# Kernel tuning notes

Measured on AMD Instinct MI355X. Metric: run time of the kernel, lower is better.

The kernel has to match this reference:

```python
import jax, jax.numpy as jnp
import numpy as np

NM = 16  # n_modes


def setup_inputs() -> dict:
    key = jax.random.key(0)
    k1, k2, k3, k4 = jax.random.split(key, 4)
    B, M, N, I, O = 8, 256, 256, 64, 64
    std = 1.0 / (I * O)
    x = jax.random.normal(k1, (B, M, N, I), dtype=jnp.float32)
    w1 = jax.random.normal(k2, (I, O, NM, NM, 2), dtype=jnp.float32) * std
    w2 = jax.random.normal(k3, (I, O, NM, NM, 2), dtype=jnp.float32) * std
    lin_w = jax.random.normal(k4, (O, O), dtype=jnp.float32) * (1.0 / np.sqrt(O))
    lin_b = jnp.zeros((O,), dtype=jnp.float32)
    return {"x": x, "w1": w1, "w2": w2, "lin_w": lin_w, "lin_b": lin_b}


def _to_complex(w):
    return jax.lax.complex(w[..., 0], w[..., 1])


def reference(x, w1, w2, lin_w, lin_b):
    B, M, N, I = x.shape
    O = w1.shape[1]
    # [B, I, M, N]
    xt = jnp.transpose(x, (0, 3, 1, 2))
    # rfft over last two dims -> [B, I, M, N//2 + 1] complex
    x_ft = jnp.fft.rfft2(xt, s=(M, N), axes=(-2, -1))
    w1c = _to_complex(w1)  # [I, O, NM, NM]
    w2c = _to_complex(w2)
    # truncated complex matmuls over low modes (top rows) and high-negative modes (bottom rows)
    out_top = jnp.einsum('bixy,ioxy->boxy', x_ft[:, :, :NM, :NM], w1c)
    out_bot = jnp.einsum('bixy,ioxy->boxy', x_ft[:, :, -NM:, :NM], w2c)
    zeros_mid = jnp.zeros((B, O, M - 2 * NM, NM), dtype=out_top.dtype)
    rows = jnp.concatenate([out_top, zeros_mid, out_bot], axis=2)  # [B, O, M, NM]
    zeros_right = jnp.zeros((B, O, M, N // 2 + 1 - NM), dtype=out_top.dtype)
    out_ft = jnp.concatenate([rows, zeros_right], axis=3)  # [B, O, M, N//2+1]
    y = jnp.fft.irfft2(out_ft, s=(M, N), axes=(-2, -1))  # real [B, O, M, N]
    y = jnp.transpose(y, (0, 2, 3, 1))  # [B, M, N, O]
    res = y @ lin_w + lin_b
    return jax.nn.relu(y + res)
```

## Files before the change

### kernel.cpp

```cpp
#include <hip/hip_runtime.h>
#include <hip/hip_bf16.h>
#include <math.h>


#define TOFF  65536
#define XOFF  (TOFF + 4194304)
#define YOFF  (XOFF + 524288)
#define GOFF  (YOFF + 524288)

__global__ __launch_bounds__(256) void setup_tables(const float* __restrict__ lin_w,
                                                    float* __restrict__ ws) {
    int j = blockIdx.x * 256 + threadIdx.x;
    const float ANG = 0.024543692606170259f;
    if (j < 4096) {
        int n = j >> 4, ky = j & 15;
        int a = (n * ky) & 255;
        float s, c; sincosf(ANG * (float)a, &s, &c);
        float* p = ws + n * 32 + ky * 2;
        p[0] = c; p[1] = -s;
    } else if (j < 12288) {
        int e = j - 4096; int m = e >> 5, kx = e & 31;
        int kxe = kx + (kx < 16 ? 0 : 224);
        int a = (m * kxe) & 255;
        float s, c; sincosf(ANG * (float)a, &s, &c);
        int g = kx >> 2, kl = kx & 3;
        float* p = ws + 8192 + g * 2048 + m * 8 + kl * 2;
        p[0] = c; p[1] = -s;
    } else if (j < 20480) {
        int e = j - 12288; int kx = e >> 8, m = e & 255;
        int kxe = kx + (kx < 16 ? 0 : 224);
        int a = (kxe * m) & 255;
        float s, c; sincosf(ANG * (float)a, &s, &c);
        float* p = ws + 24576 + (kx * 256 + m) * 2;
        p[0] = c * (1.0f / 256.0f);
        p[1] = s * (1.0f / 256.0f);
    } else if (j < 28672) {
        int e = j - 20480; int f = e >> 8, n = e & 255;
        int ky = f >> 1, h = f & 1;
        int a = (ky * n) & 255;
        float s, c; sincosf(ANG * (float)a, &s, &c);
        float scale = (ky == 0 ? 1.0f : 2.0f) * (1.0f / 256.0f);
        ws[40960 + f * 256 + n] = h ? (-scale * s) : (scale * c);
    } else if (j < 32768) {
        int e = j - 28672;
        int op = e >> 6, o = e & 63;
        ws[49152 + e] = lin_w[e] + ((op == o) ? 1.0f : 0.0f);
    }
}

__global__ __launch_bounds__(256) void stageA(const float* __restrict__ x,
                                              const float* __restrict__ tabA,
                                              float* __restrict__ T) {
    __shared__ float red[2 * 8 * 64 * 2];
    int bid = blockIdx.x;
    int b = bid >> 8, m = bid & 255;
    int t = threadIdx.x;
    int i = t & 63, w = t >> 6;
    int kh = w & 1, h = w >> 1;
    const float* xp = x + (size_t)bid * 16384 + (size_t)h * 8192 + i;
    const float* twp = tabA + __builtin_amdgcn_readfirstlane(h * 4096 + kh * 16);
    float aR[8], aI[8];
#pragma unroll
    for (int j = 0; j < 8; ++j) { aR[j] = 0.f; aI[j] = 0.f; }
#pragma unroll 4
    for (int nn = 0; nn < 128; ++nn) {
        float xv = xp[nn * 64];
        const float* tp = twp + nn * 32;
#pragma unroll
        for (int j = 0; j < 8; ++j) {
            aR[j] = fmaf(tp[2 * j], xv, aR[j]);
            aI[j] = fmaf(tp[2 * j + 1], xv, aI[j]);
        }
    }
    float2* rp = (float2*)red + (kh * 8) * 64 + i;
    if (h == 1) {
#pragma unroll
        for (int j = 0; j < 8; ++j) rp[j * 64] = make_float2(aR[j], aI[j]);
    }
    __syncthreads();
    if (h == 0) {
        float2* Tb = (float2*)T;
#pragma unroll
        for (int j = 0; j < 8; ++j) {
            float2 p = rp[j * 64];
            int ky = kh * 8 + j;
            Tb[((size_t)(b * 16 + ky) * 256 + m) * 64 + i] =
                make_float2(aR[j] + p.x, aI[j] + p.y);
        }
    }
}

__global__ __launch_bounds__(512) void stageB(const float* __restrict__ T,
                                              const float* __restrict__ twF,
                                              float* __restrict__ X) {
    __shared__ float red[4 * 4 * 64 * 2];
    int bid = blockIdx.x;
    int b = bid >> 5;
    int ky = (bid >> 1) & 15;
    int half = bid & 1;
    int t = threadIdx.x, i = t & 63;
    int q = (t >> 6) & 3, h = t >> 8;
    int Q = half * 4 + q;
    const float2* Tp = (const float2*)T + (size_t)(b * 16 + ky) * 256 * 64 + i;
    const float* tw = twF + __builtin_amdgcn_readfirstlane(Q * 2048);
    float r0 = 0, r1 = 0, r2 = 0, r3 = 0;
    float s0 = 0, s1 = 0, s2 = 0, s3 = 0;
    int m0 = h * 128;
#pragma unroll 4
    for (int mm = 0; mm < 128; ++mm) {
        int m = m0 + mm;
        float2 tv = Tp[(size_t)m * 64];
        const float* tp = tw + m * 8;
        r0 = fmaf(tv.x, tp[0], fmaf(-tv.y, tp[1], r0));
        s0 = fmaf(tv.x, tp[1], fmaf( tv.y, tp[0], s0));
        r1 = fmaf(tv.x, tp[2], fmaf(-tv.y, tp[3], r1));
        s1 = fmaf(tv.x, tp[3], fmaf( tv.y, tp[2], s1));
        r2 = fmaf(tv.x, tp[4], fmaf(-tv.y, tp[5], r2));
        s2 = fmaf(tv.x, tp[5], fmaf( tv.y, tp[4], s2));
        r3 = fmaf(tv.x, tp[6], fmaf(-tv.y, tp[7], r3));
        s3 = fmaf(tv.x, tp[7], fmaf( tv.y, tp[6], s3));
    }
    float2* rp = (float2*)red + (q * 4) * 64 + i;
    if (h == 1) {
        rp[0 * 64] = make_float2(r0, s0);
        rp[1 * 64] = make_float2(r1, s1);
        rp[2 * 64] = make_float2(r2, s2);
        rp[3 * 64] = make_float2(r3, s3);
    }
    __syncthreads();
    if (h == 0) {
        float2 p0 = rp[0 * 64], p1 = rp[1 * 64], p2 = rp[2 * 64], p3 = rp[3 * 64];
        r0 += p0.x; s0 += p0.y; r1 += p1.x; s1 += p1.y;
        r2 += p2.x; s2 += p2.y; r3 += p3.x; s3 += p3.y;
        int kx0 = Q * 4;
        float2* Xb = (float2*)X;
        size_t base = ((size_t)(b * 16 + ky) * 32 + kx0) * 64 + i;
        Xb[base + 0 * 64] = make_float2(r0, s0);
        Xb[base + 1 * 64] = make_float2(r1, s1);
        Xb[base + 2 * 64] = make_float2(r2, s2);
        Xb[base + 3 * 64] = make_float2(r3, s3);
    }
}

__global__ __launch_bounds__(256) void stageC(const float* __restrict__ Xg,
                                              const float* __restrict__ w1,
                                              const float* __restrict__ w2,
                                              const float* __restrict__ Wf,
                                              float* __restrict__ Y2) {
    __shared__ float Ws[64 * 64 * 2];
    __shared__ float Xs[8 * 64 * 2];
    __shared__ float Ys[8 * 64 * 2];
    __shared__ float Wfs[64 * 64];
    int bid = blockIdx.x;
    int kx = bid & 31, ky = bid >> 5;
    int t = threadIdx.x;
    const float* wsrc = (kx < 16) ? w1 : w2;
    int xx = kx & 15;
#pragma unroll
    for (int q = 0; q < 16; ++q) {
        int p = t + q * 256;
        int ii = p >> 6, oo = p & 63;
        float2 wv = *(const float2*)(wsrc + ((size_t)(ii * 64 + oo) * 256 + xx * 16 + ky) * 2);
        ((float2*)Ws)[ii * 64 + oo] = wv;
    }
#pragma unroll
    for (int q = 0; q < 2; ++q) {
        int p = t + q * 256;
        int bb = p >> 6, ii = p & 63;
        ((float2*)Xs)[bb * 64 + ii] =
            ((const float2*)Xg)[((size_t)(bb * 16 + ky) * 32 + kx) * 64 + ii];
    }
#pragma unroll
    for (int q = 0; q < 16; ++q) Wfs[t + q * 256] = Wf[t + q * 256];
    __syncthreads();
    int o = t & 63, bg = t >> 6;
    float yr0 = 0, yi0 = 0, yr1 = 0, yi1 = 0;
    for (int ii = 0; ii < 64; ++ii) {
        float2 w = ((float2*)Ws)[ii * 64 + o];
        float2 xa = ((float2*)Xs)[bg * 64 + ii];
        float2 xb = ((float2*)Xs)[(bg + 4) * 64 + ii];
        yr0 = fmaf(xa.x, w.x, fmaf(-xa.y, w.y, yr0));
        yi0 = fmaf(xa.x, w.y, fmaf( xa.y, w.x, yi0));
        yr1 = fmaf(xb.x, w.x, fmaf(-xb.y, w.y, yr1));
        yi1 = fmaf(xb.x, w.y, fmaf( xb.y, w.x, yi1));
    }
    ((float2*)Ys)[bg * 64 + o] = make_float2(yr0, yi0);
    ((float2*)Ys)[(bg + 4) * 64 + o] = make_float2(yr1, yi1);
    __syncthreads();
    float zr0 = 0, zi0 = 0, zr1 = 0, zi1 = 0;
    for (int op = 0; op < 64; ++op) {
        float wf = Wfs[op * 64 + o];
        float2 ya = ((float2*)Ys)[bg * 64 + op];
        float2 yb = ((float2*)Ys)[(bg + 4) * 64 + op];
        zr0 = fmaf(ya.x, wf, zr0); zi0 = fmaf(ya.y, wf, zi0);
        zr1 = fmaf(yb.x, wf, zr1); zi1 = fmaf(yb.y, wf, zi1);
    }
    float2* Yb = (float2*)Y2;
    Yb[((size_t)(bg * 32 + kx) * 16 + ky) * 64 + o] = make_float2(zr0, zi0);
    Yb[((size_t)((bg + 4) * 32 + kx) * 16 + ky) * 64 + o] = make_float2(zr1, zi1);
}

__global__ __launch_bounds__(512) void stageD(const float* __restrict__ Y2,
                                              const float* __restrict__ twI,
                                              float* __restrict__ G) {
    __shared__ float Ysl[16 * 64 * 2];
    int bid = blockIdx.x;
    int b = bid >> 5, mg = bid & 31;
    int t = threadIdx.x, o = t & 63, ml = t >> 6;
    int m = mg * 8 + ml;
    float gr[16], gi[16];
#pragma unroll
    for (int k = 0; k < 16; ++k) { gr[k] = 0.f; gi[k] = 0.f; }
    for (int kx = 0; kx < 32; ++kx) {
        __syncthreads();
        const float2* src = (const float2*)Y2 + (size_t)(b * 32 + kx) * 1024;
#pragma unroll
        for (int qq = 0; qq < 2; ++qq) ((float2*)Ysl)[t + qq * 512] = src[t + qq * 512];
        __syncthreads();
        int off = __builtin_amdgcn_readfirstlane((kx * 256 + m) * 2);
        float c = twI[off], d = twI[off + 1];
#pragma unroll
        for (int ky = 0; ky < 16; ++ky) {
            float2 yv = ((float2*)Ysl)[ky * 64 + o];
            gr[ky] = fmaf(yv.x, c, fmaf(-yv.y, d, gr[ky]));
            gi[ky] = fmaf(yv.x, d, fmaf( yv.y, c, gi[ky]));
        }
    }
    float2* Gb = (float2*)G;
#pragma unroll
    for (int ky = 0; ky < 16; ++ky)
        Gb[((size_t)(b * 256 + m) * 16 + ky) * 64 + o] = make_float2(gr[ky], gi[ky]);
}

__global__ __launch_bounds__(256) void stageE(const float* __restrict__ G,
                                              const float* __restrict__ tabE,
                                              const float* __restrict__ lin_b,
                                              float* __restrict__ out) {
    __shared__ float Bs[32 * 256];
    __shared__ float Hs[32 * 64];
    int bid = blockIdx.x;
    int t = threadIdx.x;
    const float4* tE4 = (const float4*)tabE;
#pragma unroll
    for (int q = 0; q < 8; ++q) ((float4*)Bs)[t + q * 256] = tE4[t + q * 256];
    const float2* Gp = (const float2*)G + (size_t)bid * 1024;
#pragma unroll
    for (int q = 0; q < 4; ++q) {
        int p = t + q * 256;
        int ky = p >> 6, o = p & 63;
        float2 g = Gp[p];
        Hs[(2 * ky) * 64 + o] = g.x;
        Hs[(2 * ky + 1) * 64 + o] = g.y;
    }
    __syncthreads();
    int o4 = (t & 15) * 4, n0 = (t >> 4) * 16;
    float acc[16][4];
#pragma unroll
    for (int j = 0; j < 16; ++j) { acc[j][0] = acc[j][1] = acc[j][2] = acc[j][3] = 0.f; }
    for (int f = 0; f < 32; ++f) {
        float4 h = *(const float4*)(Hs + f * 64 + o4);
        const float* bp = Bs + f * 256 + n0;
        float4 a0 = *(const float4*)(bp);
        float4 a1 = *(const float4*)(bp + 4);
        float4 a2 = *(const float4*)(bp + 8);
        float4 a3 = *(const float4*)(bp + 12);
        float av[16] = {a0.x, a0.y, a0.z, a0.w, a1.x, a1.y, a1.z, a1.w,
                        a2.x, a2.y, a2.z, a2.w, a3.x, a3.y, a3.z, a3.w};
#pragma unroll
        for (int j = 0; j < 16; ++j) {
            acc[j][0] = fmaf(av[j], h.x, acc[j][0]);
            acc[j][1] = fmaf(av[j], h.y, acc[j][1]);
            acc[j][2] = fmaf(av[j], h.z, acc[j][2]);
            acc[j][3] = fmaf(av[j], h.w, acc[j][3]);
        }
    }
    float4 bias = *(const float4*)(lin_b + o4);
    float* outp = out + (size_t)bid * 256 * 64;
#pragma unroll
    for (int j = 0; j < 16; ++j) {
        int n = n0 + j;
        float4 r;
        r.x = fmaxf(acc[j][0] + bias.x, 0.f);
        r.y = fmaxf(acc[j][1] + bias.y, 0.f);
        r.z = fmaxf(acc[j][2] + bias.z, 0.f);
        r.w = fmaxf(acc[j][3] + bias.w, 0.f);
        *(float4*)(outp + (size_t)n * 64 + o4) = r;
    }
}

extern "C" void kernel_launch(void* const* d_in, const int* in_sizes, int n_in,
                              void* d_out, int out_size, void* d_ws, size_t ws_size,
                              hipStream_t stream) {
    const float* x     = (const float*)d_in[0];
    const float* w1    = (const float*)d_in[1];
    const float* w2    = (const float*)d_in[2];
    const float* lin_w = (const float*)d_in[3];
    const float* lin_b = (const float*)d_in[4];
    float* ws  = (float*)d_ws;
    float* out = (float*)d_out;

    float* T  = ws + TOFF;
    float* X  = ws + XOFF;
    float* Y2 = ws + YOFF;
    float* G  = ws + GOFF;

    setup_tables<<<128, 256, 0, stream>>>(lin_w, ws);
    stageA<<<2048, 256, 0, stream>>>(x, ws, T);
    stageB<<<256, 512, 0, stream>>>(T, ws + 8192, X);
    stageC<<<512, 256, 0, stream>>>(X, w1, w2, ws + 49152, Y2);
    stageD<<<256, 512, 0, stream>>>(Y2, ws + 24576, G);
    stageE<<<2048, 256, 0, stream>>>(G, ws + 40960, lin_b, out);
}
```

Before: 162.3 us.

## Register-block stageA over four rows with LDS-staged twiddles

StageA now processes four m-rows per block instead of one and first copies the 32KB twiddle table into LDS, so each twiddle read is reused across four x values. This cuts the global and scalar twiddle loads per FMA and the block count drops by a factor of four. The cost is four times the accumulator registers, which can lower occupancy, and fewer blocks in flight. StageD also replaces the readfirstlane scalar twiddle load with a per-lane float2 vector load.

New measurement: 171.4 us. 1.06x slower.

```diff
diff --git a/kernel.cpp b/kernel.cpp
--- a/kernel.cpp
+++ b/kernel.cpp
@@ -51,42 +51,76 @@
 __global__ __launch_bounds__(256) void stageA(const float* __restrict__ x,
                                               const float* __restrict__ tabA,
                                               float* __restrict__ T) {
-    __shared__ float red[2 * 8 * 64 * 2];
-    int bid = blockIdx.x;
-    int b = bid >> 8, m = bid & 255;
+    __shared__ float sm[8192];
+    int bid = blockIdx.x;
+    int b = bid >> 6, mq = bid & 63;
+    int m0 = mq * 4;
     int t = threadIdx.x;
     int i = t & 63, w = t >> 6;
     int kh = w & 1, h = w >> 1;
-    const float* xp = x + (size_t)bid * 16384 + (size_t)h * 8192 + i;
-    const float* twp = tabA + __builtin_amdgcn_readfirstlane(h * 4096 + kh * 16);
-    float aR[8], aI[8];
-#pragma unroll
-    for (int j = 0; j < 8; ++j) { aR[j] = 0.f; aI[j] = 0.f; }
-#pragma unroll 4
+    {
+        const float4* src = (const float4*)tabA;
+        float4* dst = (float4*)sm;
+#pragma unroll
+        for (int q = 0; q < 8; ++q) dst[t + q * 256] = src[t + q * 256];
+    }
+    __syncthreads();
+
+    const float* xp = x + ((size_t)(b * 256 + m0) * 256 + h * 128) * 64 + i;
+    const float* twb = sm + h * 4096 + kh * 16;
+
+    float aR[4][8], aI[4][8];
+#pragma unroll
+    for (int j = 0; j < 4; ++j)
+#pragma unroll
+        for (int k = 0; k < 8; ++k) { aR[j][k] = 0.f; aI[j][k] = 0.f; }
+
+#pragma unroll 2
     for (int nn = 0; nn < 128; ++nn) {
-        float xv = xp[nn * 64];
-        const float* tp = twp + nn * 32;
-#pragma unroll
-        for (int j = 0; j < 8; ++j) {
-            aR[j] = fmaf(tp[2 * j], xv, aR[j]);
-            aI[j] = fmaf(tp[2 * j + 1], xv, aI[j]);
+        float xv0 = xp[(size_t)nn * 64];
+        float xv1 = xp[(size_t)nn * 64 + 16384];
+        float xv2 = xp[(size_t)nn * 64 + 32768];
+        float xv3 = xp[(size_t)nn * 64 + 49152];
+        const float* tp = twb + nn * 32;
+#pragma unroll
+        for (int q = 0; q < 4; ++q) {
+            float4 tv = *(const float4*)(tp + q * 4);
+            int k0 = 2 * q, k1 = 2 * q + 1;
+            aR[0][k0] = fmaf(tv.x, xv0, aR[0][k0]); aI[0][k0] = fmaf(tv.y, xv0, aI[0][k0]);
+            aR[1][k0] = fmaf(tv.x, xv1, aR[1][k0]); aI[1][k0] = fmaf(tv.y, xv1, aI[1][k0]);
+            aR[2][k0] = fmaf(tv.x, xv2, aR[2][k0]); aI[2][k0] = fmaf(tv.y, xv2, aI[2][k0]);
+            aR[3][k0] = fmaf(tv.x, xv3, aR[3][k0]); aI[3][k0] = fmaf(tv.y, xv3, aI[3][k0]);
+            aR[0][k1] = fmaf(tv.z, xv0, aR[0][k1]); aI[0][k1] = fmaf(tv.w, xv0, aI[0][k1]);
+            aR[1][k1] = fmaf(tv.z, xv1, aR[1][k1]); aI[1][k1] = fmaf(tv.w, xv1, aI[1][k1]);
+            aR[2][k1] = fmaf(tv.z, xv2, aR[2][k1]); aI[2][k1] = fmaf(tv.w, xv2, aI[2][k1]);
+            aR[3][k1] = fmaf(tv.z, xv3, aR[3][k1]); aI[3][k1] = fmaf(tv.w, xv3, aI[3][k1]);
         }
     }
-    float2* rp = (float2*)red + (kh * 8) * 64 + i;
+
+    __syncthreads();
     if (h == 1) {
-#pragma unroll
-        for (int j = 0; j < 8; ++j) rp[j * 64] = make_float2(aR[j], aI[j]);
+        float* rp = sm + kh * 4096 + i;
+#pragma unroll
+        for (int j = 0; j < 4; ++j)
+#pragma unroll
+            for (int k = 0; k < 8; ++k) {
+                rp[(j * 16 + 2 * k) * 64]     = aR[j][k];
+                rp[(j * 16 + 2 * k + 1) * 64] = aI[j][k];
+            }
     }
     __syncthreads();
     if (h == 0) {
+        const float* rp = sm + kh * 4096 + i;
         float2* Tb = (float2*)T;
 #pragma unroll
-        for (int j = 0; j < 8; ++j) {
-            float2 p = rp[j * 64];
-            int ky = kh * 8 + j;
-            Tb[((size_t)(b * 16 + ky) * 256 + m) * 64 + i] =
-                make_float2(aR[j] + p.x, aI[j] + p.y);
-        }
+        for (int j = 0; j < 4; ++j)
+#pragma unroll
+            for (int k = 0; k < 8; ++k) {
+                float r = aR[j][k] + rp[(j * 16 + 2 * k) * 64];
+                float q = aI[j][k] + rp[(j * 16 + 2 * k + 1) * 64];
+                int ky = kh * 8 + k;
+                Tb[((size_t)(b * 16 + ky) * 256 + (m0 + j)) * 64 + i] = make_float2(r, q);
+            }
     }
 }
 
@@ -217,8 +251,8 @@
 #pragma unroll
         for (int qq = 0; qq < 2; ++qq) ((float2*)Ysl)[t + qq * 512] = src[t + qq * 512];
         __syncthreads();
-        int off = __builtin_amdgcn_readfirstlane((kx * 256 + m) * 2);
-        float c = twI[off], d = twI[off + 1];
+        float2 cd = *(const float2*)(twI + (size_t)(kx * 256 + m) * 2);
+        float c = cd.x, d = cd.y;
 #pragma unroll
         for (int ky = 0; ky < 16; ++ky) {
             float2 yv = ((float2*)Ysl)[ky * 64 + o];
@@ -305,7 +339,7 @@
     float* G  = ws + GOFF;
 
     setup_tables<<<128, 256, 0, stream>>>(lin_w, ws);
-    stageA<<<2048, 256, 0, stream>>>(x, ws, T);
+    stageA<<<512, 256, 0, stream>>>(x, ws, T);
     stageB<<<256, 512, 0, stream>>>(T, ws + 8192, X);
     stageC<<<512, 256, 0, stream>>>(X, w1, w2, ws + 49152, Y2);
     stageD<<<256, 512, 0, stream>>>(Y2, ws + 24576, G);
```
